# Kernel optimization log

Hardware: AMD Instinct MI355X
Metric: run time of the kernel (lower is better)

Reference implementation:

```python
import jax, jax.numpy as jnp
import numpy as np

D_MODEL = 2048
NUM_HEADS = 16
D_K = D_MODEL // NUM_HEADS
LORA_R = 8
LORA_ALPHA = 16
SCALING = LORA_ALPHA / LORA_R  # 2.0
B, S = 2, 2048


def setup_inputs() -> dict:
    key = jax.random.key(0)
    ks = jax.random.split(key, 17)
    s = 1.0 / np.sqrt(D_MODEL)
    d = {"x": jax.random.normal(ks[0], (B, S, D_MODEL), jnp.float32)}
    i = 1
    for name in ("q", "k", "v", "o"):
        d[f"W{name}"] = jax.random.uniform(ks[i], (D_MODEL, D_MODEL), jnp.float32, -s, s); i += 1
        d[f"b{name}"] = jax.random.uniform(ks[i], (D_MODEL,), jnp.float32, -s, s); i += 1
        d[f"A{name}"] = jax.random.uniform(ks[i], (LORA_R, D_MODEL), jnp.float32, -s, s); i += 1
        # lora_B is zero-initialized in the module, but use small random so grads flow meaningfully
        d[f"B{name}"] = jax.random.normal(ks[i], (D_MODEL, LORA_R), jnp.float32) * 0.01; i += 1
    return d


def _lora_linear(x, W, b, A, Bm):
    # F.linear(x, W, b) + (x @ A.T @ B.T) * scaling
    return x @ W.T + b + ((x @ A.T) @ Bm.T) * SCALING


def reference(x, Wq, bq, Aq, Bq, Wk, bk, Ak, Bk, Wv, bv, Av, Bv, Wo, bo, Ao, Bo):
    batch = x.shape[0]
    q = _lora_linear(x, Wq, bq, Aq, Bq)
    k = _lora_linear(x, Wk, bk, Ak, Bk)
    v = _lora_linear(x, Wv, bv, Av, Bv)
    # [B, S, H, Dk] -> [B, H, S, Dk]
    q = q.reshape(batch, -1, NUM_HEADS, D_K).transpose(0, 2, 1, 3)
    k = k.reshape(batch, -1, NUM_HEADS, D_K).transpose(0, 2, 1, 3)
    v = v.reshape(batch, -1, NUM_HEADS, D_K).transpose(0, 2, 1, 3)
    scores = jnp.einsum("bhqd,bhkd->bhqk", q, k) / jnp.sqrt(jnp.float32(D_K))
    attn = jax.nn.softmax(scores, axis=-1)
    context = jnp.einsum("bhqk,bhkd->bhqd", attn, v)
    context = context.transpose(0, 2, 1, 3).reshape(batch, -1, D_MODEL)
    return _lora_linear(context, Wo, bo, Ao, Bo)
```

## Files before the change

### kernel.cpp

```cpp
#include <hip/hip_runtime.h>
#include <stdint.h>

typedef unsigned short u16;
typedef unsigned int   u32;
typedef __bf16  bf16x8 __attribute__((ext_vector_type(8)));
typedef float   f32x4  __attribute__((ext_vector_type(4)));

#define LORA_SCALE 2.0f
#define QSCALE 0.08838834764831845f
#define LOG2E  1.4426950408889634f
#define RESCALE_THR 8.0f

__device__ __forceinline__ u16 f2bf(float f){
  u32 u = __builtin_bit_cast(u32, f);
  u32 r = (u + 0x7fffu + ((u >> 16) & 1u)) >> 16;
  return (u16)r;
}
__device__ __forceinline__ float bf2f(u16 v){
  return __builtin_bit_cast(float, ((u32)v) << 16);
}
__device__ __forceinline__ u32 cvt_pk_bf16(float lo, float hi){
  u32 d;
  asm("v_cvt_pk_bf16_f32 %0, %1, %2" : "=v"(d) : "v"(lo), "v"(hi));
  return d;
}

typedef __attribute__((address_space(3))) u32 lds_u32_t;
typedef __attribute__((address_space(1))) const u32 g_u32_t;

__device__ __forceinline__ void gload16(const void* g, void* l){
  __builtin_amdgcn_global_load_lds((g_u32_t*)(unsigned long long)g,
                                   (lds_u32_t*)(u32)(unsigned long long)l,
                                   16, 0, 0);
}

__global__ __launch_bounds__(256) void cvt_w4(const float* __restrict__ W0,
    const float* __restrict__ W1, const float* __restrict__ W2,
    const float* __restrict__ W3, u16* __restrict__ wqkv, u16* __restrict__ wo){
  int sel = blockIdx.x >> 11;
  int inner = blockIdx.x & 2047;
  const float* src = sel==0 ? W0 : sel==1 ? W1 : sel==2 ? W2 : W3;
  u16* dst = sel<3 ? (wqkv + (size_t)sel*4194304) : wo;
  int i = (inner*256 + threadIdx.x) * 8;
  float4 a = *(const float4*)(src + i);
  float4 b = *(const float4*)(src + i + 4);
  u16 o[8] = {f2bf(a.x),f2bf(a.y),f2bf(a.z),f2bf(a.w),
              f2bf(b.x),f2bf(b.y),f2bf(b.z),f2bf(b.w)};
  *(uint4*)(dst + i) = *(const uint4*)o;
}

__global__ __launch_bounds__(256) void lora_x_fused(const float* __restrict__ x,
    const float* __restrict__ A0, const float* __restrict__ A1, const float* __restrict__ A2,
    float* __restrict__ xout, u16* __restrict__ xbf){
  int w = threadIdx.x >> 6, lane = threadIdx.x & 63;
  int m = blockIdx.x * 4 + w;
  float acc[3][8];
  #pragma unroll
  for (int g=0; g<3; ++g)
    #pragma unroll
    for (int r=0; r<8; ++r) acc[g][r] = 0.f;
  const float* As[3] = {A0, A1, A2};
  #pragma unroll 1
  for (int it=0; it<8; ++it){
    int k = it*256 + lane*4;
    float4 xv = *(const float4*)(x + (size_t)m*2048 + k);
    u16 o[4] = {f2bf(xv.x), f2bf(xv.y), f2bf(xv.z), f2bf(xv.w)};
    *(uint2*)(xbf + (size_t)m*2048 + k) = *(const uint2*)o;
    #pragma unroll
    for (int g=0; g<3; ++g){
      const float* Ag = As[g];
      #pragma unroll
      for (int r=0; r<8; ++r){
        float4 av = *(const float4*)(Ag + r*2048 + k);
        acc[g][r] += xv.x*av.x + xv.y*av.y + xv.z*av.z + xv.w*av.w;
      }
    }
  }
  #pragma unroll
  for (int g=0; g<3; ++g)
    #pragma unroll
    for (int r=0; r<8; ++r){
      float v = acc[g][r];
      #pragma unroll
      for (int off=32; off; off>>=1) v += __shfl_xor(v, off);
      if (lane == 0) xout[g*32768 + m*8 + r] = v;
    }
}

__global__ __launch_bounds__(256) void lora_xa_bf16(const u16* __restrict__ xin,
    const float* __restrict__ A0, float* __restrict__ xout){
  int w = threadIdx.x >> 6, lane = threadIdx.x & 63;
  int m = blockIdx.x * 4 + w;
  float acc[8];
  #pragma unroll
  for (int r=0; r<8; ++r) acc[r] = 0.f;
  #pragma unroll 1
  for (int it=0; it<8; ++it){
    int k = it*256 + lane*4;
    ushort4 u = *(const ushort4*)(xin + (size_t)m*2048 + k);
    float4 xv = {bf2f(u.x), bf2f(u.y), bf2f(u.z), bf2f(u.w)};
    #pragma unroll
    for (int r=0; r<8; ++r){
      float4 av = *(const float4*)(A0 + r*2048 + k);
      acc[r] += xv.x*av.x + xv.y*av.y + xv.z*av.z + xv.w*av.w;
    }
  }
  #pragma unroll
  for (int r=0; r<8; ++r){
    float v = acc[r];
    #pragma unroll
    for (int off=32; off; off>>=1) v += __shfl_xor(v, off);
    if (lane == 0) xout[m*8 + r] = v;
  }
}

__device__ __forceinline__ void gemm_core_256(
    const u16* __restrict__ Aptr,
    const u16* __restrict__ Wptr,
    u16* lds, int tid, f32x4 acc[4][4]){
  const int Kd = 2048;
  int l = tid & 63, w = tid >> 6;
  int l15 = l & 15, l4 = l >> 4;
  int wm = w >> 1, wn = w & 1;
  int srow = w*16 + (l >> 2);
  int scol = ((l & 3) ^ ((l >> 3) & 3)) * 8;
  const u16* asrc0 = Aptr + (size_t)srow * Kd + scol;
  const u16* asrc1 = asrc0 + (size_t)128 * Kd;
  const u16* bsrc  = Wptr + (size_t)srow * Kd + scol;
  char* L = (char*)lds;
  int wb = w * 1024;

  int rsw = ((l4 ^ ((l15 >> 1) & 3)) << 4);
  int abase = (wm*64 + l15)*64 + rsw;
  int bbase = 16384 + (wn*64 + l15)*64 + rsw;

  #define STAGE_A(t) { int bb_ = ((t)&3)*24576; \
      gload16(asrc0 + (t)*32, L + bb_ + wb); \
      gload16(asrc1 + (t)*32, L + bb_ + 8192 + wb); }
  #define STAGE_B(t) { int bb_ = ((t)&3)*24576; \
      gload16(bsrc + (t)*32, L + bb_ + 16384 + wb); }

  STAGE_A(0); STAGE_B(0); STAGE_A(1); STAGE_B(1); STAGE_A(2); STAGE_B(2);
  asm volatile("s_waitcnt vmcnt(6)" ::: "memory");
  __builtin_amdgcn_s_barrier();

  #pragma unroll 1
  for (int t = 0; t < 64; ++t){
    int bb = (t & 3) * 24576;
    bf16x8 bf[4], af0, af1;
    af0 = *(const bf16x8*)(L + bb + abase);
    af1 = *(const bf16x8*)(L + bb + abase + 1024);
    #pragma unroll
    for (int nr=0; nr<4; ++nr) bf[nr] = *(const bf16x8*)(L + bb + bbase + nr*1024);
    if (t < 61) STAGE_A(t+3);
    __builtin_amdgcn_s_barrier();
    __builtin_amdgcn_s_setprio(1);
    #pragma unroll
    for (int nr=0; nr<4; ++nr){
      acc[0][nr] = __builtin_amdgcn_mfma_f32_16x16x32_bf16(af0, bf[nr], acc[0][nr], 0, 0, 0);
      acc[1][nr] = __builtin_amdgcn_mfma_f32_16x16x32_bf16(af1, bf[nr], acc[1][nr], 0, 0, 0);
    }
    __builtin_amdgcn_s_setprio(0);
    __builtin_amdgcn_s_barrier();
    af0 = *(const bf16x8*)(L + bb + abase + 2048);
    af1 = *(const bf16x8*)(L + bb + abase + 3072);
    if (t < 61){
      STAGE_B(t+3);
      asm volatile("s_waitcnt vmcnt(6)" ::: "memory");
    } else if (t == 61){
      asm volatile("s_waitcnt vmcnt(3)" ::: "memory");
    } else if (t == 62){
      asm volatile("s_waitcnt vmcnt(0)" ::: "memory");
    }
    __builtin_amdgcn_s_barrier();
    __builtin_amdgcn_s_setprio(1);
    #pragma unroll
    for (int nr=0; nr<4; ++nr){
      acc[2][nr] = __builtin_amdgcn_mfma_f32_16x16x32_bf16(af0, bf[nr], acc[2][nr], 0, 0, 0);
      acc[3][nr] = __builtin_amdgcn_mfma_f32_16x16x32_bf16(af1, bf[nr], acc[3][nr], 0, 0, 0);
    }
    __builtin_amdgcn_s_setprio(0);
    __builtin_amdgcn_s_barrier();
  }
  #undef STAGE_A
  #undef STAGE_B
}

__global__ __launch_bounds__(512, 2) void gemm_qkv(
    const u16* __restrict__ A, const u16* __restrict__ W,
    const float* __restrict__ bq, const float* __restrict__ bk, const float* __restrict__ bv,
    const float* __restrict__ lBq, const float* __restrict__ lBk, const float* __restrict__ lBv,
    const float* __restrict__ xa, u16* __restrict__ Qb, u16* __restrict__ Kb, u16* __restrict__ Vb){
  __shared__ u16 lds[49152];
  int tid = threadIdx.x;
  int l = tid & 63, w = tid >> 6;
  int l15 = l & 15, l4 = l >> 4;
  int wm = w >> 1, wn = w & 1;
  int bid = blockIdx.x;
  int virt = (bid & 7) * 96 + (bid >> 3);
  int mt = virt & 15, nt = virt >> 4;
  int m0 = mt * 256, n0g = nt * 128;
  int which = nt >> 4;
  int n0 = (nt & 15) * 128;
  const float* bias = which==0 ? bq : which==1 ? bk : bv;
  const float* lB   = which==0 ? lBq : which==1 ? lBk : lBv;
  const float* xs   = xa + which*32768;
  u16* outp         = which==0 ? Qb : which==1 ? Kb : Vb;
  int swz = (which <= 1);
  float oscale = (which == 0) ? QSCALE*LOG2E : 1.0f;

  f32x4 acc[4][4];
  #pragma unroll
  for (int mr=0; mr<4; mr++)
    #pragma unroll
    for (int nr=0; nr<4; nr++) acc[mr][nr] = (f32x4){0.f,0.f,0.f,0.f};

  gemm_core_256(A + (size_t)m0*2048, W + (size_t)n0g*2048, lds, tid, acc);

  float bvv[4]; float4 lb0[4], lb1[4];
  #pragma unroll
  for (int nr=0; nr<4; nr++){
    int col = n0 + wn*64 + nr*16 + l15;
    bvv[nr] = bias[col];
    lb0[nr] = *(const float4*)(lB + col*8);
    lb1[nr] = *(const float4*)(lB + col*8 + 4);
  }
  #pragma unroll
  for (int mr=0; mr<4; mr++)
    #pragma unroll
    for (int j=0; j<4; j++){
      int r = m0 + wm*64 + mr*16 + l4*4 + j;
      float4 xv0 = *(const float4*)(xs + (size_t)r*8);
      float4 xv1 = *(const float4*)(xs + (size_t)r*8 + 4);
      #pragma unroll
      for (int nr=0; nr<4; nr++){
        int col = n0 + wn*64 + nr*16 + l15;
        float v = acc[mr][nr][j] + bvv[nr] + LORA_SCALE * (
            xv0.x*lb0[nr].x + xv0.y*lb0[nr].y + xv0.z*lb0[nr].z + xv0.w*lb0[nr].w +
            xv1.x*lb1[nr].x + xv1.y*lb1[nr].y + xv1.z*lb1[nr].z + xv1.w*lb1[nr].w);
        v *= oscale;
        int cs = swz ? (col ^ ((r & 7) << 3)) : col;
        outp[(size_t)r*2048 + cs] = f2bf(v);
      }
    }
}

__global__ __launch_bounds__(512, 2) void gemm_o(
    const u16* __restrict__ A, const u16* __restrict__ W,
    const float* __restrict__ bias, const float* __restrict__ lB,
    const float* __restrict__ xa, float* __restrict__ outp){
  __shared__ u16 lds[49152];
  int tid = threadIdx.x;
  int l = tid & 63, w = tid >> 6;
  int l15 = l & 15, l4 = l >> 4;
  int wm = w >> 1, wn = w & 1;
  int bid = blockIdx.x;
  int virt = (bid & 7) * 32 + (bid >> 3);
  int mt = virt & 15, nt = virt >> 4;
  int m0 = mt * 256, n0 = nt * 128;

  f32x4 acc[4][4];
  #pragma unroll
  for (int mr=0; mr<4; mr++)
    #pragma unroll
    for (int nr=0; nr<4; nr++) acc[mr][nr] = (f32x4){0.f,0.f,0.f,0.f};

  gemm_core_256(A + (size_t)m0*2048, W + (size_t)n0*2048, lds, tid, acc);

  float bv[4]; float4 lb0[4], lb1[4];
  #pragma unroll
  for (int nr=0; nr<4; nr++){
    int col = n0 + wn*64 + nr*16 + l15;
    bv[nr] = bias[col];
    lb0[nr] = *(const float4*)(lB + col*8);
    lb1[nr] = *(const float4*)(lB + col*8 + 4);
  }
  #pragma unroll
  for (int mr=0; mr<4; mr++)
    #pragma unroll
    for (int j=0; j<4; j++){
      int r = m0 + wm*64 + mr*16 + l4*4 + j;
      float4 xv0 = *(const float4*)(xa + (size_t)r*8);
      float4 xv1 = *(const float4*)(xa + (size_t)r*8 + 4);
      #pragma unroll
      for (int nr=0; nr<4; nr++){
        int col = n0 + wn*64 + nr*16 + l15;
        float v = acc[mr][nr][j] + bv[nr] + LORA_SCALE * (
            xv0.x*lb0[nr].x + xv0.y*lb0[nr].y + xv0.z*lb0[nr].z + xv0.w*lb0[nr].w +
            xv1.x*lb1[nr].x + xv1.y*lb1[nr].y + xv1.z*lb1[nr].z + xv1.w*lb1[nr].w);
        outp[(size_t)r*2048 + col] = v;
      }
    }
}

__global__ __launch_bounds__(256) void transpose_v(const u16* __restrict__ V,
                                                   u16* __restrict__ Vt){
  __shared__ u16 tile[64*80];
  int tid = threadIdx.x;
  int f0 = blockIdx.x * 64, m0 = blockIdx.y * 64;
  int i = tid >> 2, j0 = (tid & 3) * 16;
  #pragma unroll
  for (int kk=0; kk<16; kk+=8){
    uint4 u = *(const uint4*)(V + (size_t)(m0 + i)*2048 + f0 + j0 + kk);
    *(uint4*)(tile + i*80 + j0 + kk) = u;
  }
  __syncthreads();
  int j = tid >> 2, i0 = (tid & 3) * 16;
  int b = m0 >> 11, s0 = m0 & 2047;
  int h = f0 >> 7, d = (f0 & 127) + j;
  int c = (d & 7) << 3;
  size_t obase = ((size_t)((b*16 + h)*128 + d)) * 2048 + s0;
  #pragma unroll
  for (int kk=0; kk<16; kk+=8){
    u16 v8[8];
    #pragma unroll
    for (int u2=0; u2<8; ++u2) v8[u2] = tile[(i0+kk+u2)*80 + j];
    *(uint4*)(Vt + obase + ((i0+kk) ^ c)) = *(const uint4*)v8;
  }
}

__global__ __launch_bounds__(256, 2) void attn_kernel(
    const u16* __restrict__ Q, const u16* __restrict__ K,
    const u16* __restrict__ Vt, u16* __restrict__ ctx){
  __shared__ u16 buf[2][16384];
  __shared__ u16 Psh[4*32*64];
  int tid = threadIdx.x, w = tid >> 6, lane = tid & 63;
  int l15 = lane & 15, l4 = lane >> 4;
  int lin = blockIdx.x;
  int virt = (lin & 7) * 64 + (lin >> 3);
  int qt = virt & 15, bh = virt >> 4;
  int b = bh >> 4, h = bh & 15;
  const u16* Qg = Q + (size_t)(b*2048 + qt*128) * 2048 + h*128;
  const u16* Kg = K + (size_t)(b*2048) * 2048 + h*128;
  const u16* Vg = Vt + (size_t)bh * 128 * 2048;

  #pragma unroll
  for (int i=0; i<8; ++i){
    int e = (i*256 + tid) * 8;
    int r = e >> 7, cc = e & 127;
    gload16(Qg + (size_t)r*2048 + cc, (char*)buf[1] + i*4096 + w*1024);
  }
  #pragma unroll
  for (int i=0; i<4; ++i){
    int e = (i*256 + tid) * 8;
    int r = e >> 7, cc = e & 127;
    gload16(Kg + (size_t)r*2048 + cc, (char*)buf[0] + i*4096 + w*1024);
    int dd = e >> 6, c2 = e & 63;
    gload16(Vg + (size_t)dd*2048 + c2, (char*)buf[0] + 16384 + i*4096 + w*1024);
  }
  __syncthreads();

  bf16x8 qf[2][4];
  #pragma unroll
  for (int mi=0; mi<2; mi++){
    int r = w*32 + mi*16 + l15;
    #pragma unroll
    for (int kb=0; kb<4; kb++){
      int cc = (kb*32 + l4*8) ^ ((r & 7) << 3);
      qf[mi][kb] = *(const bf16x8*)(buf[1] + r*128 + cc);
    }
  }
  __syncthreads();

  f32x4 ctxa[2][8];
  #pragma unroll
  for (int mi=0; mi<2; mi++)
    #pragma unroll
    for (int nd=0; nd<8; nd++) ctxa[mi][nd] = (f32x4){0.f,0.f,0.f,0.f};
  float mrun[2] = {-3.0e38f, -3.0e38f};
  float lrun[2] = {0.f, 0.f};

  char* PwB = (char*)(Psh + w * (32*64));
  int psw = (l15 & 7) << 4;

  for (int t = 0; t < 32; ++t){
    int cur = t & 1;
    const u16* Kc = buf[cur];
    const u16* Vc = buf[cur] + 8192;
    if (t + 1 < 32){
      int kvn = (t + 1) * 64;
      char* bn = (char*)buf[cur ^ 1];
      #pragma unroll
      for (int i=0; i<4; ++i){
        int e = (i*256 + tid) * 8;
        int r = e >> 7, cc = e & 127;
        gload16(Kg + (size_t)(kvn + r)*2048 + cc, bn + i*4096 + w*1024);
        int dd = e >> 6, c2 = e & 63;
        gload16(Vg + (size_t)dd*2048 + kvn + c2, bn + 16384 + i*4096 + w*1024);
      }
    }
    f32x4 s[2][4];
    #pragma unroll
    for (int mi=0; mi<2; mi++)
      #pragma unroll
      for (int ni=0; ni<4; ni++) s[mi][ni] = (f32x4){0.f,0.f,0.f,0.f};
    __builtin_amdgcn_s_setprio(1);
    #pragma unroll
    for (int kb=0; kb<4; kb++){
      #pragma unroll
      for (int ni=0; ni<4; ni++){
        int r = ni*16 + l15;
        int cc = (kb*32 + l4*8) ^ ((r & 7) << 3);
        bf16x8 kf = *(const bf16x8*)(Kc + r*128 + cc);
        s[0][ni] = __builtin_amdgcn_mfma_f32_16x16x32_bf16(kf, qf[0][kb], s[0][ni], 0, 0, 0);
        s[1][ni] = __builtin_amdgcn_mfma_f32_16x16x32_bf16(kf, qf[1][kb], s[1][ni], 0, 0, 0);
      }
    }
    __builtin_amdgcn_s_setprio(0);
    float pm[2];
    #pragma unroll
    for (int mi=0; mi<2; mi++){
      float v = s[mi][0][0];
      #pragma unroll
      for (int ni=0; ni<4; ni++)
        #pragma unroll
        for (int j=0; j<4; j++) v = fmaxf(v, s[mi][ni][j]);
      v = fmaxf(v, __shfl_xor(v, 16));
      v = fmaxf(v, __shfl_xor(v, 32));
      pm[mi] = v;
    }
    bool need = (pm[0] > mrun[0] + RESCALE_THR) || (pm[1] > mrun[1] + RESCALE_THR);
    if (__any(need)){
      #pragma unroll
      for (int mi=0; mi<2; mi++){
        float mnew = fmaxf(mrun[mi], pm[mi]);
        float cr = exp2f(mrun[mi] - mnew);
        lrun[mi] *= cr;
        mrun[mi] = mnew;
        #pragma unroll
        for (int nd=0; nd<8; nd++) ctxa[mi][nd] *= cr;
      }
    }
    #pragma unroll
    for (int mi=0; mi<2; mi++){
      float ps = 0.f;
      #pragma unroll
      for (int ni=0; ni<4; ni++){
        float p0 = exp2f(s[mi][ni][0] - mrun[mi]);
        float p1 = exp2f(s[mi][ni][1] - mrun[mi]);
        float p2 = exp2f(s[mi][ni][2] - mrun[mi]);
        float p3 = exp2f(s[mi][ni][3] - mrun[mi]);
        ps += (p0 + p1) + (p2 + p3);
        uint2 pk = {cvt_pk_bf16(p0, p1), cvt_pk_bf16(p2, p3)};
        *(uint2*)(PwB + (mi*16 + l15)*128 + ((ni*32 + l4*8) ^ psw)) = pk;
      }
      ps += __shfl_xor(ps, 16);
      ps += __shfl_xor(ps, 32);
      lrun[mi] += ps;
    }
    bf16x8 pb[2][2];
    #pragma unroll
    for (int mi=0; mi<2; mi++)
      #pragma unroll
      for (int kvb=0; kvb<2; kvb++)
        pb[mi][kvb] = *(const bf16x8*)(PwB + (mi*16 + l15)*128 + ((kvb*64 + l4*16) ^ psw));
    __builtin_amdgcn_s_setprio(1);
    #pragma unroll
    for (int nd=0; nd<8; nd++){
      int dd = nd*16 + l15;
      int sw = (dd & 7) << 3;
      #pragma unroll
      for (int kvb=0; kvb<2; kvb++){
        bf16x8 vf = *(const bf16x8*)(Vc + dd*64 + ((kvb*32 + l4*8) ^ sw));
        ctxa[0][nd] = __builtin_amdgcn_mfma_f32_16x16x32_bf16(vf, pb[0][kvb], ctxa[0][nd], 0, 0, 0);
        ctxa[1][nd] = __builtin_amdgcn_mfma_f32_16x16x32_bf16(vf, pb[1][kvb], ctxa[1][nd], 0, 0, 0);
      }
    }
    __builtin_amdgcn_s_setprio(0);
    __syncthreads();
  }
  char* OwB = (char*)buf[0] + w*8192;
  #pragma unroll
  for (int mi=0; mi<2; mi++){
    float inv = 1.0f / lrun[mi];
    #pragma unroll
    for (int nd=0; nd<8; nd++){
      f32x4 c = ctxa[mi][nd] * inv;
      uint2 pk = {cvt_pk_bf16(c[0], c[1]), cvt_pk_bf16(c[2], c[3])};
      *(uint2*)(OwB + (mi*16 + l15)*256 + ((nd*32 + l4*8) ^ psw)) = pk;
    }
  }
  #pragma unroll
  for (int i=0; i<8; ++i){
    int row = i*4 + l4;
    int colb = l15*16;
    uint4 v = *(const uint4*)(OwB + row*256 + (colb ^ ((row & 7) << 4)));
    int srow = qt*128 + w*32 + row;
    *(uint4*)(ctx + ((size_t)(b*2048 + srow))*2048 + h*128 + colb/2) = v;
  }
}

extern "C" void kernel_launch(void* const* d_in, const int* in_sizes, int n_in,
                              void* d_out, int out_size, void* d_ws, size_t ws_size,
                              hipStream_t stream){
  const float* x  = (const float*)d_in[0];
  const float* Wq = (const float*)d_in[1];  const float* bq = (const float*)d_in[2];
  const float* Aq = (const float*)d_in[3];  const float* Bq = (const float*)d_in[4];
  const float* Wk = (const float*)d_in[5];  const float* bk = (const float*)d_in[6];
  const float* Ak = (const float*)d_in[7];  const float* Bk = (const float*)d_in[8];
  const float* Wv = (const float*)d_in[9];  const float* bv = (const float*)d_in[10];
  const float* Av = (const float*)d_in[11]; const float* Bv = (const float*)d_in[12];
  const float* Wo = (const float*)d_in[13]; const float* bo = (const float*)d_in[14];
  const float* Ao = (const float*)d_in[15]; const float* Bo = (const float*)d_in[16];

  char* ws = (char*)d_ws;
  size_t off = 0;
  u16* xbf  = (u16*)(ws + off); off += (size_t)4096*2048*2;
  u16* wqkv = (u16*)(ws + off); off += (size_t)3*2048*2048*2;
  u16* wob  = (u16*)(ws + off); off += (size_t)2048*2048*2;
  float* xa = (float*)(ws + off); off += (size_t)4*32768*4;
  u16* Qb  = (u16*)(ws + off); off += (size_t)4096*2048*2;
  u16* Kb  = (u16*)(ws + off); off += (size_t)4096*2048*2;
  u16* Vb  = (u16*)(ws + off); off += (size_t)4096*2048*2;
  u16* Vtb = (u16*)(ws + off); off += (size_t)4096*2048*2;
  if (ws_size < off) return;

  cvt_w4<<<8192, 256, 0, stream>>>(Wq, Wk, Wv, Wo, wqkv, wob);
  lora_x_fused<<<1024, 256, 0, stream>>>(x, Aq, Ak, Av, xa, xbf);

  gemm_qkv<<<768, 512, 0, stream>>>(xbf, wqkv, bq, bk, bv, Bq, Bk, Bv, xa, Qb, Kb, Vb);

  transpose_v<<<dim3(32,64), 256, 0, stream>>>(Vb, Vtb);

  attn_kernel<<<512, 256, 0, stream>>>(Qb, Kb, Vtb, Vb);

  lora_xa_bf16<<<1024, 256, 0, stream>>>(Vb, Ao, xa+98304);

  gemm_o<<<256, 512, 0, stream>>>(Vb, wob, bo, Bo, xa+98304, (float*)d_out);
}
```

Before: 355.0 us.

## Use 4-wave GEMM blocks with 8x4 MFMA tiles and 3-stage LDS ring

The shared GEMM core moves from 8 waves per 256x128 tile to 4 waves, each computing a 128x64 sub-tile with 8x4 accumulators. This doubles the register reuse of each LDS fragment. The LDS pipeline shrinks from 4 stages to a 3-stage ring buffer, which frees shared memory per block, and the staging loads are issued all at once per k-step. The cost is higher per-thread register pressure and fewer waves to hide latency.

```diff
diff --git a/kernel.cpp b/kernel.cpp
--- a/kernel.cpp
+++ b/kernel.cpp
@@ -114,84 +114,87 @@
   }
 }
 
-__device__ __forceinline__ void gemm_core_256(
+__device__ __forceinline__ void gemm_core_v7(
     const u16* __restrict__ Aptr,
     const u16* __restrict__ Wptr,
-    u16* lds, int tid, f32x4 acc[4][4]){
+    u16* lds, int tid, f32x4 acc[8][4]){
   const int Kd = 2048;
   int l = tid & 63, w = tid >> 6;
   int l15 = l & 15, l4 = l >> 4;
   int wm = w >> 1, wn = w & 1;
-  int srow = w*16 + (l >> 2);
-  int scol = ((l & 3) ^ ((l >> 3) & 3)) * 8;
-  const u16* asrc0 = Aptr + (size_t)srow * Kd + scol;
-  const u16* asrc1 = asrc0 + (size_t)128 * Kd;
-  const u16* bsrc  = Wptr + (size_t)srow * Kd + scol;
   char* L = (char*)lds;
   int wb = w * 1024;
-
-  int rsw = ((l4 ^ ((l15 >> 1) & 3)) << 4);
-  int abase = (wm*64 + l15)*64 + rsw;
-  int bbase = 16384 + (wn*64 + l15)*64 + rsw;
-
-  #define STAGE_A(t) { int bb_ = ((t)&3)*24576; \
-      gload16(asrc0 + (t)*32, L + bb_ + wb); \
-      gload16(asrc1 + (t)*32, L + bb_ + 8192 + wb); }
-  #define STAGE_B(t) { int bb_ = ((t)&3)*24576; \
-      gload16(bsrc + (t)*32, L + bb_ + 16384 + wb); }
-
-  STAGE_A(0); STAGE_B(0); STAGE_A(1); STAGE_B(1); STAGE_A(2); STAGE_B(2);
+  const u16* asrc[4]; const u16* bsrc[2];
+  #pragma unroll
+  for (int i=0;i<4;i++){ int row=(i*4+w)*16+(l>>2); int sc=((l&3)^((row>>1)&3))<<3;
+    asrc[i] = Aptr + (size_t)row*Kd + sc; }
+  #pragma unroll
+  for (int i=0;i<2;i++){ int row=(i*4+w)*16+(l>>2); int sc=((l&3)^((row>>1)&3))<<3;
+    bsrc[i] = Wptr + (size_t)row*Kd + sc; }
+  int aoff[8], boff[4];
+  #pragma unroll
+  for (int mr=0;mr<8;mr++){ int ra=wm*128+mr*16+l15; aoff[mr]=ra*64+((l4^((ra>>1)&3))<<4); }
+  #pragma unroll
+  for (int nr=0;nr<4;nr++){ int rb=wn*64+nr*16+l15; boff[nr]=16384+rb*64+((l4^((rb>>1)&3))<<4); }
+
+  auto STG = [&](int kt, int sbase){
+    char* D = L + sbase;
+    gload16(asrc[0]+kt, D +        wb);
+    gload16(asrc[1]+kt, D +  4096+ wb);
+    gload16(asrc[2]+kt, D +  8192+ wb);
+    gload16(asrc[3]+kt, D + 12288+ wb);
+    gload16(bsrc[0]+kt, D + 16384+ wb);
+    gload16(bsrc[1]+kt, D + 20480+ wb);
+  };
+
+  STG(0, 0); STG(32, 24576);
   asm volatile("s_waitcnt vmcnt(6)" ::: "memory");
   __builtin_amdgcn_s_barrier();
 
+  int bb = 0, sb = 49152, kt2 = 64;
   #pragma unroll 1
   for (int t = 0; t < 64; ++t){
-    int bb = (t & 3) * 24576;
-    bf16x8 bf[4], af0, af1;
-    af0 = *(const bf16x8*)(L + bb + abase);
-    af1 = *(const bf16x8*)(L + bb + abase + 1024);
-    #pragma unroll
-    for (int nr=0; nr<4; ++nr) bf[nr] = *(const bf16x8*)(L + bb + bbase + nr*1024);
-    if (t < 61) STAGE_A(t+3);
+    bf16x8 af[4], bf[4];
+    #pragma unroll
+    for (int mr=0;mr<4;mr++) af[mr] = *(const bf16x8*)(L + bb + aoff[mr]);
+    #pragma unroll
+    for (int nr=0;nr<4;nr++) bf[nr] = *(const bf16x8*)(L + bb + boff[nr]);
+    if (t < 62) STG(kt2, sb);
     __builtin_amdgcn_s_barrier();
     __builtin_amdgcn_s_setprio(1);
     #pragma unroll
-    for (int nr=0; nr<4; ++nr){
-      acc[0][nr] = __builtin_amdgcn_mfma_f32_16x16x32_bf16(af0, bf[nr], acc[0][nr], 0, 0, 0);
-      acc[1][nr] = __builtin_amdgcn_mfma_f32_16x16x32_bf16(af1, bf[nr], acc[1][nr], 0, 0, 0);
-    }
+    for (int mr=0;mr<4;mr++)
+      #pragma unroll
+      for (int nr=0;nr<4;nr++)
+        acc[mr][nr] = __builtin_amdgcn_mfma_f32_16x16x32_bf16(af[mr], bf[nr], acc[mr][nr], 0,0,0);
     __builtin_amdgcn_s_setprio(0);
     __builtin_amdgcn_s_barrier();
-    af0 = *(const bf16x8*)(L + bb + abase + 2048);
-    af1 = *(const bf16x8*)(L + bb + abase + 3072);
-    if (t < 61){
-      STAGE_B(t+3);
-      asm volatile("s_waitcnt vmcnt(6)" ::: "memory");
-    } else if (t == 61){
-      asm volatile("s_waitcnt vmcnt(3)" ::: "memory");
-    } else if (t == 62){
-      asm volatile("s_waitcnt vmcnt(0)" ::: "memory");
-    }
+    bf16x8 ag[4];
+    #pragma unroll
+    for (int mr=0;mr<4;mr++) ag[mr] = *(const bf16x8*)(L + bb + aoff[mr+4]);
+    if (t < 62)       asm volatile("s_waitcnt vmcnt(6)" ::: "memory");
+    else if (t == 62) asm volatile("s_waitcnt vmcnt(0)" ::: "memory");
     __builtin_amdgcn_s_barrier();
     __builtin_amdgcn_s_setprio(1);
     #pragma unroll
-    for (int nr=0; nr<4; ++nr){
-      acc[2][nr] = __builtin_amdgcn_mfma_f32_16x16x32_bf16(af0, bf[nr], acc[2][nr], 0, 0, 0);
-      acc[3][nr] = __builtin_amdgcn_mfma_f32_16x16x32_bf16(af1, bf[nr], acc[3][nr], 0, 0, 0);
-    }
+    for (int mr=0;mr<4;mr++)
+      #pragma unroll
+      for (int nr=0;nr<4;nr++)
+        acc[mr+4][nr] = __builtin_amdgcn_mfma_f32_16x16x32_bf16(ag[mr], bf[nr], acc[mr+4][nr], 0,0,0);
     __builtin_amdgcn_s_setprio(0);
     __builtin_amdgcn_s_barrier();
-  }
-  #undef STAGE_A
-  #undef STAGE_B
-}
-
-__global__ __launch_bounds__(512, 2) void gemm_qkv(
+    bb = (bb == 49152) ? 0 : bb + 24576;
+    sb = (sb == 49152) ? 0 : sb + 24576;
+    kt2 += 32;
+  }
+}
+
+__global__ __launch_bounds__(256, 2) void gemm_qkv(
     const u16* __restrict__ A, const u16* __restrict__ W,
     const float* __restrict__ bq, const float* __restrict__ bk, const float* __restrict__ bv,
     const float* __restrict__ lBq, const float* __restrict__ lBk, const float* __restrict__ lBv,
     const float* __restrict__ xa, u16* __restrict__ Qb, u16* __restrict__ Kb, u16* __restrict__ Vb){
-  __shared__ u16 lds[49152];
+  __shared__ u16 lds[36864];
   int tid = threadIdx.x;
   int l = tid & 63, w = tid >> 6;
   int l15 = l & 15, l4 = l >> 4;
@@ -209,13 +212,13 @@
   int swz = (which <= 1);
   float oscale = (which == 0) ? QSCALE*LOG2E : 1.0f;
 
-  f32x4 acc[4][4];
-  #pragma unroll
-  for (int mr=0; mr<4; mr++)
+  f32x4 acc[8][4];
+  #pragma unroll
+  for (int mr=0; mr<8; mr++)
     #pragma unroll
     for (int nr=0; nr<4; nr++) acc[mr][nr] = (f32x4){0.f,0.f,0.f,0.f};
 
-  gemm_core_256(A + (size_t)m0*2048, W + (size_t)n0g*2048, lds, tid, acc);
+  gemm_core_v7(A + (size_t)m0*2048, W + (size_t)n0g*2048, lds, tid, acc);
 
   float bvv[4]; float4 lb0[4], lb1[4];
   #pragma unroll
@@ -226,10 +229,10 @@
     lb1[nr] = *(const float4*)(lB + col*8 + 4);
   }
   #pragma unroll
-  for (int mr=0; mr<4; mr++)
+  for (int mr=0; mr<8; mr++)
     #pragma unroll
     for (int j=0; j<4; j++){
-      int r = m0 + wm*64 + mr*16 + l4*4 + j;
+      int r = m0 + wm*128 + mr*16 + l4*4 + j;
       float4 xv0 = *(const float4*)(xs + (size_t)r*8);
       float4 xv1 = *(const float4*)(xs + (size_t)r*8 + 4);
       #pragma unroll
@@ -245,11 +248,11 @@
     }
 }
 
-__global__ __launch_bounds__(512, 2) void gemm_o(
+__global__ __launch_bounds__(256, 2) void gemm_o(
     const u16* __restrict__ A, const u16* __restrict__ W,
     const float* __restrict__ bias, const float* __restrict__ lB,
     const float* __restrict__ xa, float* __restrict__ outp){
-  __shared__ u16 lds[49152];
+  __shared__ u16 lds[36864];
   int tid = threadIdx.x;
   int l = tid & 63, w = tid >> 6;
   int l15 = l & 15, l4 = l >> 4;
@@ -259,13 +262,13 @@
   int mt = virt & 15, nt = virt >> 4;
   int m0 = mt * 256, n0 = nt * 128;
 
-  f32x4 acc[4][4];
-  #pragma unroll
-  for (int mr=0; mr<4; mr++)
+  f32x4 acc[8][4];
+  #pragma unroll
+  for (int mr=0; mr<8; mr++)
     #pragma unroll
     for (int nr=0; nr<4; nr++) acc[mr][nr] = (f32x4){0.f,0.f,0.f,0.f};
 
-  gemm_core_256(A + (size_t)m0*2048, W + (size_t)n0*2048, lds, tid, acc);
+  gemm_core_v7(A + (size_t)m0*2048, W + (size_t)n0*2048, lds, tid, acc);
 
   float bv[4]; float4 lb0[4], lb1[4];
   #pragma unroll
@@ -276,10 +279,10 @@
     lb1[nr] = *(const float4*)(lB + col*8 + 4);
   }
   #pragma unroll
-  for (int mr=0; mr<4; mr++)
+  for (int mr=0; mr<8; mr++)
     #pragma unroll
     for (int j=0; j<4; j++){
-      int r = m0 + wm*64 + mr*16 + l4*4 + j;
+      int r = m0 + wm*128 + mr*16 + l4*4 + j;
       float4 xv0 = *(const float4*)(xa + (size_t)r*8);
       float4 xv1 = *(const float4*)(xa + (size_t)r*8 + 4);
       #pragma unroll
@@ -518,7 +521,7 @@
   cvt_w4<<<8192, 256, 0, stream>>>(Wq, Wk, Wv, Wo, wqkv, wob);
   lora_x_fused<<<1024, 256, 0, stream>>>(x, Aq, Ak, Av, xa, xbf);
 
-  gemm_qkv<<<768, 512, 0, stream>>>(xbf, wqkv, bq, bk, bv, Bq, Bk, Bv, xa, Qb, Kb, Vb);
+  gemm_qkv<<<768, 256, 0, stream>>>(xbf, wqkv, bq, bk, bv, Bq, Bk, Bv, xa, Qb, Kb, Vb);
 
   transpose_v<<<dim3(32,64), 256, 0, stream>>>(Vb, Vtb);
 
@@ -526,5 +529,5 @@
 
   lora_xa_bf16<<<1024, 256, 0, stream>>>(Vb, Ao, xa+98304);
 
-  gemm_o<<<256, 512, 0, stream>>>(Vb, wob, bo, Bo, xa+98304, (float*)d_out);
-}
+  gemm_o<<<256, 256, 0, stream>>>(Vb, wob, bo, Bo, xa+98304, (float*)d_out);
+}
```

New measurement: 339.9 us. -4.2%, faster.
